# Kernel tuning notes

Hardware: AMD Instinct MI355X
Metric: run time of the kernel (lower is better)

Reference implementation:

```python
import jax, jax.numpy as jnp
import numpy as np

N, E, DIN, DOUT = 100000, 500000, 256, 1


def setup_inputs() -> dict:
    key = jax.random.key(0)
    k1, k2, k3, k4 = jax.random.split(key, 4)
    x = jax.random.normal(k1, (N, DIN), dtype=jnp.float32)
    edge_label_index = jax.random.randint(k2, (2, E), 0, N, dtype=jnp.int64)
    # nn.Linear default init: U(-1/sqrt(fan_in), 1/sqrt(fan_in)); plain scaled normal is fine for a numeric reference
    W1 = jax.random.normal(k3, (2 * DIN, DIN), dtype=jnp.float32) / np.sqrt(2 * DIN)
    b1 = jnp.zeros((DIN,), dtype=jnp.float32)
    W2 = jax.random.normal(k4, (DIN, DOUT), dtype=jnp.float32) / np.sqrt(DIN)
    b2 = jnp.zeros((DOUT,), dtype=jnp.float32)
    return {"x": x, "edge_label_index": edge_label_index, "W1": W1, "b1": b1, "W2": W2, "b2": b2}


def reference(x, edge_label_index, W1, b1, W2, b2):
    x_i = x[edge_label_index[0]]            # [E, DIN] gather src
    x_j = x[edge_label_index[1]]            # [E, DIN] gather dst
    h = jnp.concatenate([x_i, x_j], axis=-1)  # [E, 2*DIN]
    h = jax.nn.relu(h @ W1 + b1)            # [E, DIN]
    return h @ W2 + b2                      # [E, DOUT]
```

## Files before the change

kernel.cpp:

```cpp
#include <hip/hip_runtime.h>
#include <hip/hip_bf16.h>


typedef short short8 __attribute__((ext_vector_type(8)));
typedef float f32x4 __attribute__((ext_vector_type(4)));

#define DINC 256
#define NOUTC 512

__device__ inline unsigned short f2bf(float f) {
  union { float f; unsigned u; } c; c.f = f;
  unsigned u = c.u;
  return (unsigned short)((u + 0x7FFFu + ((u >> 16) & 1u)) >> 16);
}
__device__ inline float bf2f(unsigned short h) {
  union { unsigned u; float f; } c; c.u = ((unsigned)h) << 16;
  return c.f;
}
__device__ inline unsigned short fbf(float f) {
  union { __hip_bfloat16 h; unsigned short u; } c;
  c.h = __float2bfloat16(f);
  return c.u;
}

__global__ void w1t_kernel(const float* __restrict__ W1, unsigned short* __restrict__ W1t) {
  int t = blockIdx.x * 256 + threadIdx.x;
  int lane = t & 63, nf = (t >> 6) & 7, kt = (t >> 9) & 7, bn = t >> 12;
  int col = bn * 128 + nf * 16 + (lane & 15);
  int k0 = kt * 32 + (lane >> 4) * 8;
  int off = (col >= 256) ? 256 : 0;
  int cs = col & 255;
  short8 v;
#pragma unroll
  for (int j = 0; j < 8; ++j)
    v[j] = (short)f2bf(W1[(size_t)(k0 + j + off) * DINC + cs]);
  *(short8*)(W1t + (size_t)t * 8) = v;
}

__global__ __launch_bounds__(256, 1) void uv_gemm(const float* __restrict__ x,
                                                  const unsigned short* __restrict__ W1t,
                                                  unsigned short* __restrict__ uv,
                                                  int Nn) {
  __shared__ unsigned short Bs[128 * DINC];

  int L = (blockIdx.x & 7) * (gridDim.x >> 3) + (blockIdx.x >> 3);
  int bn = L & 3, rank = L >> 2;

  int tid = threadIdx.x, lane = tid & 63, w = tid >> 6;
  int lr = lane & 15, kg = lane >> 4;

  {
    const char* bsrc = (const char*)W1t + (size_t)bn * 65536;
#pragma unroll
    for (int i = 0; i < 16; ++i) {
      int o = i * 4096 + w * 1024;
      __builtin_amdgcn_global_load_lds(
          (const __attribute__((address_space(1))) void*)(bsrc + o + lane * 16),
          (__attribute__((address_space(3))) void*)((char*)Bs + o), 16, 0, 0);
    }
  }
  __syncthreads();

  int nch = (Nn + 15) >> 4;
  int stream = rank * 4 + w;
  const int S = 512;

#define LOADH(BUF, C)                                                          \
  {                                                                            \
    int row_ = (C) * 16 + lr;                                                  \
    if (row_ >= Nn) row_ = Nn - 1;                                             \
    const float4* xp_ = (const float4*)(x + (size_t)row_ * DINC + kg * 8);     \
    _Pragma("unroll")                                                          \
    for (int kt = 0; kt < 8; ++kt) {                                           \
      BUF[2 * kt]     = xp_[kt * 8];                                           \
      BUF[2 * kt + 1] = xp_[kt * 8 + 1];                                       \
    }                                                                          \
  }

#define CS(BUF, C)                                                             \
  {                                                                            \
    f32x4 acc[8] = {};                                                         \
    _Pragma("unroll")                                                          \
    for (int kt = 0; kt < 8; ++kt) {                                           \
      float4 f0 = BUF[2 * kt], f1 = BUF[2 * kt + 1];                           \
      short8 a;                                                                \
      a[0] = (short)fbf(f0.x); a[1] = (short)fbf(f0.y);                        \
      a[2] = (short)fbf(f0.z); a[3] = (short)fbf(f0.w);                        \
      a[4] = (short)fbf(f1.x); a[5] = (short)fbf(f1.y);                        \
      a[6] = (short)fbf(f1.z); a[7] = (short)fbf(f1.w);                        \
      _Pragma("unroll")                                                        \
      for (int nf = 0; nf < 8; ++nf) {                                         \
        short8 bf_ = *(const short8*)((char*)Bs + ((kt * 8 + nf) * 64 + lane) * 16); \
        acc[nf] = __builtin_amdgcn_mfma_f32_16x16x32_bf16(bf_, a,              \
                                                          acc[nf], 0, 0, 0);   \
      }                                                                        \
    }                                                                          \
    int row_ = (C) * 16 + lr;                                                  \
    if (row_ < Nn) {                                                           \
      unsigned short* orow_ = uv + (size_t)row_ * NOUTC + bn * 128 + kg * 4;   \
      _Pragma("unroll")                                                        \
      for (int nf = 0; nf < 8; ++nf) {                                         \
        ushort4 pk;                                                            \
        pk.x = fbf(acc[nf][0]); pk.y = fbf(acc[nf][1]);                        \
        pk.z = fbf(acc[nf][2]); pk.w = fbf(acc[nf][3]);                        \
        *(ushort4*)(orow_ + nf * 16) = pk;                                     \
      }                                                                        \
    }                                                                          \
  }

  float4 A0[16], A1[16];
  int c = stream;
  if (c < nch) {
    LOADH(A0, c);
    for (;;) {
      int c1 = c + S;
      if (c1 < nch) {
        LOADH(A1, c1);
        CS(A0, c);
        int c2 = c1 + S;
        if (c2 < nch) {
          LOADH(A0, c2);
          CS(A1, c1);
          c = c2;
        } else { CS(A1, c1); break; }
      } else { CS(A0, c); break; }
    }
  }
#undef LOADH
#undef CS
}

__global__ __launch_bounds__(256) void edge_kernel(const int* __restrict__ eliW,
                                                   const unsigned short* __restrict__ uv,
                                                   const float* __restrict__ b1,
                                                   const float* __restrict__ W2,
                                                   const float* __restrict__ b2,
                                                   float* __restrict__ out, int E) {
  int tid = threadIdx.x;
  int ql = tid & 15;
  bool is64 = ((eliW[1] | eliW[3] | eliW[5] | eliW[7] | eliW[9] | eliW[11]) == 0);
  int shift = is64 ? 1 : 0;

  float bl[16], wl[16];
  *(float4*)(bl + 0)  = *(const float4*)(b1 + ql * 8);
  *(float4*)(bl + 4)  = *(const float4*)(b1 + ql * 8 + 4);
  *(float4*)(bl + 8)  = *(const float4*)(b1 + 128 + ql * 8);
  *(float4*)(bl + 12) = *(const float4*)(b1 + 128 + ql * 8 + 4);
  *(float4*)(wl + 0)  = *(const float4*)(W2 + ql * 8);
  *(float4*)(wl + 4)  = *(const float4*)(W2 + ql * 8 + 4);
  *(float4*)(wl + 8)  = *(const float4*)(W2 + 128 + ql * 8);
  *(float4*)(wl + 12) = *(const float4*)(W2 + 128 + ql * 8 + 4);
  float bias2 = b2[0];

  int qid = (blockIdx.x * blockDim.x + tid) >> 4;
  int nq = (gridDim.x * blockDim.x) >> 4;

#define DOT(UU, VV, SREG)                                                      \
  {                                                                            \
    float s_ = 0.f;                                                            \
    _Pragma("unroll")                                                          \
    for (int g = 0; g < 2; ++g)                                                \
      _Pragma("unroll")                                                        \
      for (int j = 0; j < 8; ++j) {                                            \
        float h = bf2f((unsigned short)UU[g][j]) +                             \
                  bf2f((unsigned short)VV[g][j]) + bl[g * 8 + j];              \
        s_ += fmaxf(h, 0.f) * wl[g * 8 + j];                                   \
      }                                                                        \
    _Pragma("unroll")                                                          \
    for (int off = 8; off; off >>= 1) s_ += __shfl_xor(s_, off, 64);           \
    SREG = s_;                                                                 \
  }

  for (int e = qid; e < E; e += 2 * nq) {
    int e1 = e + nq;
    bool has1 = e1 < E;
    int e1c = has1 ? e1 : e;
    int src0 = eliW[((size_t)e) << shift];
    int dst0 = eliW[((size_t)(E + e)) << shift];
    int src1 = eliW[((size_t)e1c) << shift];
    int dst1 = eliW[((size_t)(E + e1c)) << shift];

    const unsigned short* up0 = uv + (size_t)src0 * NOUTC;
    const unsigned short* vp0 = uv + (size_t)dst0 * NOUTC + DINC;
    const unsigned short* up1 = uv + (size_t)src1 * NOUTC;
    const unsigned short* vp1 = uv + (size_t)dst1 * NOUTC + DINC;

    short8 uu0[2], vv0[2], uu1[2], vv1[2];
    uu0[0] = *(const short8*)(up0 + ql * 8);
    uu0[1] = *(const short8*)(up0 + 128 + ql * 8);
    vv0[0] = *(const short8*)(vp0 + ql * 8);
    vv0[1] = *(const short8*)(vp0 + 128 + ql * 8);
    uu1[0] = *(const short8*)(up1 + ql * 8);
    uu1[1] = *(const short8*)(up1 + 128 + ql * 8);
    vv1[0] = *(const short8*)(vp1 + ql * 8);
    vv1[1] = *(const short8*)(vp1 + 128 + ql * 8);

    float s0, s1;
    DOT(uu0, vv0, s0);
    DOT(uu1, vv1, s1);
    if (ql == 0) {
      out[e] = s0 + bias2;
      if (has1) out[e1] = s1 + bias2;
    }
  }
#undef DOT
}

extern "C" void kernel_launch(void* const* d_in, const int* in_sizes, int n_in,
                              void* d_out, int out_size, void* d_ws, size_t ws_size,
                              hipStream_t stream) {
  const float* x   = (const float*)d_in[0];
  const int*   eli = (const int*)d_in[1];
  const float* W1  = (const float*)d_in[2];
  const float* b1  = (const float*)d_in[3];
  const float* W2  = (const float*)d_in[4];
  const float* b2  = (const float*)d_in[5];
  float* out = (float*)d_out;

  int Nn = in_sizes[0] / DINC;
  int E  = in_sizes[1] / 2;

  unsigned short* W1t = (unsigned short*)d_ws;
  unsigned short* uv  = W1t + (size_t)NOUTC * DINC;

  w1t_kernel<<<64, 256, 0, stream>>>(W1, W1t);

  uv_gemm<<<512, 256, 0, stream>>>(x, W1t, uv, Nn);

  edge_kernel<<<2048, 256, 0, stream>>>(eli, uv, b1, W2, b2, out, E);
}
```

Measured before the change: 161.0 us.

## Pre-convert x to bf16 fragment layout and process 32-row chunks in GEMM

Adds a separate kernel that converts x from fp32 to bf16 and stores it already laid out as MFMA A-fragments. The projection GEMM then loads those fragments directly, with no per-element conversion, and handles 32 rows per chunk with two accumulator sets. This reuses each LDS B-fragment read for two MFMAs. The cost is an extra full pass over x: an fp32 read plus a bf16 write and re-read, and one more kernel launch. It also needs more workspace and more registers.

```diff
diff --git a/kernel.cpp b/kernel.cpp
--- a/kernel.cpp
+++ b/kernel.cpp
@@ -37,7 +37,25 @@
   *(short8*)(W1t + (size_t)t * 8) = v;
 }
 
-__global__ __launch_bounds__(256, 1) void uv_gemm(const float* __restrict__ x,
+__global__ __launch_bounds__(256) void cvt_kernel(const float* __restrict__ x,
+                                                  unsigned short* __restrict__ xbf,
+                                                  int Nn) {
+  int g = blockIdx.x * 256 + threadIdx.x;
+  int lane = g & 63, kt = (g >> 6) & 7, c = g >> 9;
+  int row = c * 16 + (lane & 15);
+  if (row >= Nn) row = Nn - 1;
+  int k0 = kt * 32 + (lane >> 4) * 8;
+  const float4* xp = (const float4*)(x + (size_t)row * DINC + k0);
+  float4 f0 = xp[0], f1 = xp[1];
+  short8 v;
+  v[0] = (short)fbf(f0.x); v[1] = (short)fbf(f0.y);
+  v[2] = (short)fbf(f0.z); v[3] = (short)fbf(f0.w);
+  v[4] = (short)fbf(f1.x); v[5] = (short)fbf(f1.y);
+  v[6] = (short)fbf(f1.z); v[7] = (short)fbf(f1.w);
+  *(short8*)(xbf + (size_t)g * 8) = v;
+}
+
+__global__ __launch_bounds__(256, 1) void uv_gemm(const unsigned short* __restrict__ xbf,
                                                   const unsigned short* __restrict__ W1t,
                                                   unsigned short* __restrict__ uv,
                                                   int Nn) {
@@ -61,54 +79,60 @@
   }
   __syncthreads();
 
-  int nch = (Nn + 15) >> 4;
+  int nch = (Nn + 31) >> 5;
   int stream = rank * 4 + w;
   const int S = 512;
+  const char* xb = (const char*)xbf;
 
 #define LOADH(BUF, C)                                                          \
   {                                                                            \
-    int row_ = (C) * 16 + lr;                                                  \
-    if (row_ >= Nn) row_ = Nn - 1;                                             \
-    const float4* xp_ = (const float4*)(x + (size_t)row_ * DINC + kg * 8);     \
+    const char* p_ = xb + (size_t)(2 * (C)) * 8192 + lane * 16;                \
     _Pragma("unroll")                                                          \
     for (int kt = 0; kt < 8; ++kt) {                                           \
-      BUF[2 * kt]     = xp_[kt * 8];                                           \
-      BUF[2 * kt + 1] = xp_[kt * 8 + 1];                                       \
+      BUF[kt]     = *(const short8*)(p_ + kt * 1024);                          \
+      BUF[8 + kt] = *(const short8*)(p_ + 8192 + kt * 1024);                   \
     }                                                                          \
   }
 
 #define CS(BUF, C)                                                             \
   {                                                                            \
-    f32x4 acc[8] = {};                                                         \
+    f32x4 acc0[8] = {}, acc1[8] = {};                                          \
     _Pragma("unroll")                                                          \
     for (int kt = 0; kt < 8; ++kt) {                                           \
-      float4 f0 = BUF[2 * kt], f1 = BUF[2 * kt + 1];                           \
-      short8 a;                                                                \
-      a[0] = (short)fbf(f0.x); a[1] = (short)fbf(f0.y);                        \
-      a[2] = (short)fbf(f0.z); a[3] = (short)fbf(f0.w);                        \
-      a[4] = (short)fbf(f1.x); a[5] = (short)fbf(f1.y);                        \
-      a[6] = (short)fbf(f1.z); a[7] = (short)fbf(f1.w);                        \
       _Pragma("unroll")                                                        \
       for (int nf = 0; nf < 8; ++nf) {                                         \
         short8 bf_ = *(const short8*)((char*)Bs + ((kt * 8 + nf) * 64 + lane) * 16); \
-        acc[nf] = __builtin_amdgcn_mfma_f32_16x16x32_bf16(bf_, a,              \
-                                                          acc[nf], 0, 0, 0);   \
-      }                                                                        \
-    }                                                                          \
-    int row_ = (C) * 16 + lr;                                                  \
-    if (row_ < Nn) {                                                           \
-      unsigned short* orow_ = uv + (size_t)row_ * NOUTC + bn * 128 + kg * 4;   \
+        acc0[nf] = __builtin_amdgcn_mfma_f32_16x16x32_bf16(bf_, BUF[kt],       \
+                                                           acc0[nf], 0, 0, 0); \
+        acc1[nf] = __builtin_amdgcn_mfma_f32_16x16x32_bf16(bf_, BUF[8 + kt],   \
+                                                           acc1[nf], 0, 0, 0); \
+      }                                                                        \
+    }                                                                          \
+    int row0_ = (C) * 32 + lr;                                                 \
+    if (row0_ < Nn) {                                                          \
+      unsigned short* orow_ = uv + (size_t)row0_ * NOUTC + bn * 128 + kg * 4;  \
       _Pragma("unroll")                                                        \
       for (int nf = 0; nf < 8; ++nf) {                                         \
         ushort4 pk;                                                            \
-        pk.x = fbf(acc[nf][0]); pk.y = fbf(acc[nf][1]);                        \
-        pk.z = fbf(acc[nf][2]); pk.w = fbf(acc[nf][3]);                        \
+        pk.x = fbf(acc0[nf][0]); pk.y = fbf(acc0[nf][1]);                      \
+        pk.z = fbf(acc0[nf][2]); pk.w = fbf(acc0[nf][3]);                      \
         *(ushort4*)(orow_ + nf * 16) = pk;                                     \
       }                                                                        \
     }                                                                          \
-  }
-
-  float4 A0[16], A1[16];
+    int row1_ = row0_ + 16;                                                    \
+    if (row1_ < Nn) {                                                          \
+      unsigned short* orow_ = uv + (size_t)row1_ * NOUTC + bn * 128 + kg * 4;  \
+      _Pragma("unroll")                                                        \
+      for (int nf = 0; nf < 8; ++nf) {                                         \
+        ushort4 pk;                                                            \
+        pk.x = fbf(acc1[nf][0]); pk.y = fbf(acc1[nf][1]);                      \
+        pk.z = fbf(acc1[nf][2]); pk.w = fbf(acc1[nf][3]);                      \
+        *(ushort4*)(orow_ + nf * 16) = pk;                                     \
+      }                                                                        \
+    }                                                                          \
+  }
+
+  short8 A0[16], A1[16];
   int c = stream;
   if (c < nch) {
     LOADH(A0, c);
@@ -219,13 +243,16 @@
 
   int Nn = in_sizes[0] / DINC;
   int E  = in_sizes[1] / 2;
+  int nch16 = (Nn + 15) >> 4;
 
   unsigned short* W1t = (unsigned short*)d_ws;
   unsigned short* uv  = W1t + (size_t)NOUTC * DINC;
+  unsigned short* xbf = uv + (size_t)Nn * NOUTC;
 
   w1t_kernel<<<64, 256, 0, stream>>>(W1, W1t);
-
-  uv_gemm<<<512, 256, 0, stream>>>(x, W1t, uv, Nn);
+  cvt_kernel<<<nch16 * 2, 256, 0, stream>>>(x, xbf, Nn);
+
+  uv_gemm<<<512, 256, 0, stream>>>(xbf, W1t, uv, Nn);
 
   edge_kernel<<<2048, 256, 0, stream>>>(eli, uv, b1, W2, b2, out, E);
 }
```

After: 148.5 us. -7.8%, faster.
